# Kernel tuning notes

Hardware: AMD Instinct MI355X
Metric: run time of the kernel (lower is better)

Reference implementation:

```python
import jax, jax.numpy as jnp
import numpy as np

EMBED = 1024
HEADS = 16
HEAD_DIM = EMBED // HEADS


def setup_inputs() -> dict:
    key = jax.random.key(0)
    ks = jax.random.split(key, 8)
    N, L = 2, 2048
    s = 0.02
    return {
        "values": jax.random.normal(ks[0], (N, L, EMBED), jnp.float32),
        "keys": jax.random.normal(ks[1], (N, L, EMBED), jnp.float32),
        "queries": jax.random.normal(ks[2], (N, L, EMBED), jnp.float32),
        "Wv": jax.random.normal(ks[3], (HEAD_DIM, HEAD_DIM), jnp.float32) * s,
        "Wk": jax.random.normal(ks[4], (HEAD_DIM, HEAD_DIM), jnp.float32) * s,
        "Wq": jax.random.normal(ks[5], (HEAD_DIM, HEAD_DIM), jnp.float32) * s,
        "Wo": jax.random.normal(ks[6], (EMBED, EMBED), jnp.float32) * s,
        "bo": jnp.zeros((EMBED,), jnp.float32),
    }


def reference(values, keys, queries, Wv, Wk, Wq, Wo, bo):
    N, Lq = queries.shape[0], queries.shape[1]
    Lk = keys.shape[1]
    Lv = values.shape[1]
    # split heads: [N, L, H, D]
    v = values.reshape(N, Lv, HEADS, HEAD_DIM)
    k = keys.reshape(N, Lk, HEADS, HEAD_DIM)
    q = queries.reshape(N, Lq, HEADS, HEAD_DIM)
    # per-head linear projections (torch Linear: x @ W.T), shared across heads
    v = jnp.einsum('nlhd,ed->nlhe', v, Wv)
    k = jnp.einsum('nlhd,ed->nlhe', k, Wk)
    q = jnp.einsum('nlhd,ed->nlhe', q, Wq)
    # attention scores [N, H, Lq, Lk]
    scores = jnp.einsum('nqhd,nkhd->nhqk', q, k) / jnp.sqrt(jnp.float32(HEAD_DIM))
    attn = jax.nn.softmax(scores, axis=-1)
    out = jnp.einsum('nhql,nlhd->nqhd', attn, v).reshape(N, Lq, EMBED)
    return out @ Wo.T + bo
```

## Files before the change

kernel.cpp:

```cpp
#include <hip/hip_runtime.h>
#include <hip/hip_bf16.h>
#include <cstdint>
#include <cstddef>

#define HEADS 16
#define HDIM  64
#define EMBED 1024
#define SEQ   2048
#define NB    2

typedef __attribute__((ext_vector_type(8))) short short8;
typedef __attribute__((ext_vector_type(4))) short s16x4;
typedef __attribute__((ext_vector_type(4))) float f32x4;
typedef __attribute__((ext_vector_type(16))) float f32x16;

__device__ __forceinline__ short f2bf(float f) {
    union { float f; uint32_t u; } in{f};
    uint32_t u = in.u;
    u += 0x7fffu + ((u >> 16) & 1u);
    return (short)(u >> 16);
}

__device__ __forceinline__ int cvtpk(float a, float b) {
    __hip_bfloat162 h = __float22bfloat162_rn(make_float2(a, b));
    int i;
    __builtin_memcpy(&i, &h, 4);
    return i;
}

__device__ __forceinline__ short8 load_cvt8(const float* __restrict__ p) {
    const f32x4* q = (const f32x4*)p;
    f32x4 v0 = q[0], v1 = q[1];
    short8 r;
    r[0] = f2bf(v0[0]); r[1] = f2bf(v0[1]); r[2] = f2bf(v0[2]); r[3] = f2bf(v0[3]);
    r[4] = f2bf(v1[0]); r[5] = f2bf(v1[1]); r[6] = f2bf(v1[2]); r[7] = f2bf(v1[3]);
    return r;
}

__global__ __launch_bounds__(256) void wcvt_kernel(
    const float* __restrict__ Wq, const float* __restrict__ Wk,
    const float* __restrict__ Wv, const float* __restrict__ Wo,
    short* __restrict__ Wqb, short* __restrict__ Wkb,
    short* __restrict__ Wvb, short* __restrict__ Wob) {
    int b = blockIdx.x, tid = threadIdx.x;
    if (b < 1024) {
        int o = b * 1024 + tid * 4;
        int page = o >> 9, inp = o & 511;
        int nb = page >> 5, kb = page & 31;
        int lp = inp >> 3, jj = inp & 7;
        int row = nb * 16 + (lp & 15);
        int colf = kb * 32 + (lp >> 4) * 8 + jj;
        f32x4 v = *(const f32x4*)(Wo + row * 1024 + colf);
        s16x4 r;
        r[0] = f2bf(v[0]); r[1] = f2bf(v[1]); r[2] = f2bf(v[2]); r[3] = f2bf(v[3]);
        *(s16x4*)(Wob + o) = r;
    } else {
        const float* src = (b == 1024) ? Wq : (b == 1025) ? Wk : Wv;
        short* dst = (b == 1024) ? Wqb : (b == 1025) ? Wkb : Wvb;
        float scale = (b == 1024) ? 0.125f * 1.44269504088896341f : 1.0f;
#pragma unroll
        for (int k = 0; k < 4; ++k) {
            int idx = tid * 16 + k * 4;
            f32x4 v = *(const f32x4*)(src + idx);
            s16x4 r;
            r[0] = f2bf(v[0] * scale); r[1] = f2bf(v[1] * scale);
            r[2] = f2bf(v[2] * scale); r[3] = f2bf(v[3] * scale);
            *(s16x4*)(dst + idx) = r;
        }
    }
}

__global__ __launch_bounds__(256) void proj_kernel(
    const float* __restrict__ qrys, const float* __restrict__ keys,
    const float* __restrict__ vals,
    const short* __restrict__ Wqb, const short* __restrict__ Wkb,
    const short* __restrict__ Wvb,
    short* __restrict__ Qp, short* __restrict__ Kf, short* __restrict__ Vf) {
    __shared__ short tile[64][72];
    int tid = threadIdx.x, lane = tid & 63, w = tid >> 6;
    int g = lane >> 4, c = lane & 15;
    int tt = blockIdx.x * 64;
    int h = blockIdx.y;
    int z = blockIdx.z;
    int op = z >> 1, n = z & 1;
    int nh = n * 16 + h;
    const float* src = (op == 0) ? qrys : (op == 1) ? keys : vals;
    const short* Wb = (op == 0) ? Wqb : (op == 1) ? Wkb : Wvb;

    int lt0 = tt + w * 16;
    const float* sp_ = src + ((size_t)(n * SEQ + lt0 + c) * 16 + h) * 64;
    short8 a0 = load_cvt8(sp_ + 8 * g);
    short8 a1 = load_cvt8(sp_ + 32 + 8 * g);
#pragma unroll
    for (int ot = 0; ot < 4; ++ot) {
        short8 b0 = *(const short8*)(Wb + (ot * 16 + c) * 64 + 8 * g);
        short8 b1 = *(const short8*)(Wb + (ot * 16 + c) * 64 + 32 + 8 * g);
        f32x4 acc = {0.f, 0.f, 0.f, 0.f};
        acc = __builtin_amdgcn_mfma_f32_16x16x32_bf16(a0, b0, acc, 0, 0, 0);
        acc = __builtin_amdgcn_mfma_f32_16x16x32_bf16(a1, b1, acc, 0, 0, 0);
        if (op == 2) {
#pragma unroll
            for (int r = 0; r < 4; ++r)
                tile[ot * 16 + c][w * 16 + 4 * g + r] = f2bf(acc[r]);
        } else {
#pragma unroll
            for (int r = 0; r < 4; ++r)
                tile[w * 16 + 4 * g + r][ot * 16 + c] = f2bf(acc[r]);
        }
    }
    __syncthreads();
    if (op == 0) {
#pragma unroll
        for (int it = 0; it < 2; ++it) {
            int idx = tid + it * 256;
            int row = idx >> 3, ch = idx & 7;
            short8 v = *(const short8*)(&tile[row][ch * 8]);
            *(short8*)(Qp + ((size_t)nh * SEQ + tt + row) * 64 + ch * 8) = v;
        }
    } else {
        short* dst = (op == 1) ? Kf : Vf;
        int spx = tt >> 10;
        int tbase = (tt >> 5) & 31;
        size_t grp = (size_t)(nh * 2 + spx) * 32;
#pragma unroll
        for (int it = 0; it < 2; ++it) {
            int idx = tid + it * 256;
            int tl2 = idx >> 8;
            int p = (idx >> 6) & 3;
            int ln = idx & 63;
            int hi2 = ln >> 5, col2 = ln & 31;
            const short* srcp;
            if (op == 1) {
                srcp = &tile[tl2 * 32 + col2][p * 16 + hi2 * 8];
            } else {
                srcp = &tile[(p & 1) * 32 + col2][tl2 * 32 + (p >> 1) * 16 + hi2 * 8];
            }
            *(short8*)(dst + ((grp + tbase + tl2) * 4 + p) * 512 + ln * 8) =
                *(const short8*)srcp;
        }
    }
}

__global__ __launch_bounds__(256, 4) void attn_kernel(
    const short* __restrict__ Qp, const short* __restrict__ Kf,
    const short* __restrict__ Vf, short* __restrict__ X) {
    __shared__ float obuf[2][32][64];
    __shared__ float larr[2][2][32];

    int tid = threadIdx.x, lane = tid & 63, wave = tid >> 6;
    int col = lane & 31, hi = lane >> 5;
    int qg = wave >> 1, sp = wave & 1;

    int lid = blockIdx.x;
    int xcd = lid & 7, idx = lid >> 3;
    int nh = xcd * 4 + (idx & 3);
    int qb = idx >> 2;
    int n = nh >> 4, h = nh & 15;
    int q0w = qb * 64 + qg * 32;

    const short* Qb = Qp + (size_t)nh * SEQ * 64;
    const short* Kw = Kf + (((size_t)(nh * 2 + sp)) << 16) + lane * 8;
    const short* Vw = Vf + (((size_t)(nh * 2 + sp)) << 16) + lane * 8;

    short8 qf[4];
#pragma unroll
    for (int t = 0; t < 4; ++t)
        qf[t] = *(const short8*)(Qb + (size_t)(q0w + col) * 64 + 16 * t + 8 * hi);

    f32x16 o0, o1;
#pragma unroll
    for (int r = 0; r < 16; ++r) { o0[r] = 0.f; o1[r] = 0.f; }
    float la = 0.f, lb = 0.f;

#pragma unroll 1
    for (int t = 0; t < 32; ++t) {
        short8 kf[4], vf[4];
#pragma unroll
        for (int dt = 0; dt < 4; ++dt)
            kf[dt] = *(const short8*)(Kw + ((size_t)(t * 4 + dt) << 9));
#pragma unroll
        for (int p = 0; p < 4; ++p)
            vf[p] = *(const short8*)(Vw + ((size_t)(t * 4 + p) << 9));

        f32x16 s;
#pragma unroll
        for (int r = 0; r < 16; ++r) s[r] = 0.f;
#pragma unroll
        for (int dt = 0; dt < 4; ++dt)
            s = __builtin_amdgcn_mfma_f32_32x32x16_bf16(kf[dt], qf[dt], s, 0, 0, 0);

#pragma unroll
        for (int r = 0; r < 16; r += 2) {
            s[r] = __builtin_amdgcn_exp2f(s[r]);
            s[r + 1] = __builtin_amdgcn_exp2f(s[r + 1]);
            la += s[r];
            lb += s[r + 1];
        }
        int pk0 = cvtpk(s[0], s[1]),   pk1 = cvtpk(s[2], s[3]);
        int pk2 = cvtpk(s[4], s[5]),   pk3 = cvtpk(s[6], s[7]);
        int pk4 = cvtpk(s[8], s[9]),   pk5 = cvtpk(s[10], s[11]);
        int pk6 = cvtpk(s[12], s[13]), pk7 = cvtpk(s[14], s[15]);
        auto r02 = __builtin_amdgcn_permlane32_swap(pk0, pk2, false, false);
        auto r13 = __builtin_amdgcn_permlane32_swap(pk1, pk3, false, false);
        auto r46 = __builtin_amdgcn_permlane32_swap(pk4, pk6, false, false);
        auto r57 = __builtin_amdgcn_permlane32_swap(pk5, pk7, false, false);
        union { int i[4]; short8 s8; } pa0, pa1;
        pa0.i[0] = r02[0]; pa0.i[1] = r13[0]; pa0.i[2] = r02[1]; pa0.i[3] = r13[1];
        pa1.i[0] = r46[0]; pa1.i[1] = r57[0]; pa1.i[2] = r46[1]; pa1.i[3] = r57[1];
        o0 = __builtin_amdgcn_mfma_f32_32x32x16_bf16(pa0.s8, vf[0], o0, 0, 0, 0);
        o1 = __builtin_amdgcn_mfma_f32_32x32x16_bf16(pa0.s8, vf[1], o1, 0, 0, 0);
        o0 = __builtin_amdgcn_mfma_f32_32x32x16_bf16(pa1.s8, vf[2], o0, 0, 0, 0);
        o1 = __builtin_amdgcn_mfma_f32_32x32x16_bf16(pa1.s8, vf[3], o1, 0, 0, 0);
    }

    float l_loc = la + lb;
    l_loc += __shfl_xor(l_loc, 32);

    if (lane < 32) larr[qg][sp][col] = l_loc;
    if (sp == 0) {
#pragma unroll
        for (int r = 0; r < 16; ++r) {
            int rq = (r & 3) + 8 * (r >> 2) + 4 * hi;
            obuf[qg][rq][col] = o0[r];
            obuf[qg][rq][32 + col] = o1[r];
        }
    }
    __syncthreads();
    if (sp == 1) {
#pragma unroll
        for (int r = 0; r < 16; ++r) {
            int rq = (r & 3) + 8 * (r >> 2) + 4 * hi;
            float ltot = larr[qg][0][rq] + larr[qg][1][rq];
            float iv = 1.0f / ltot;
            float v0 = o0[r] + obuf[qg][rq][col];
            float v1 = o1[r] + obuf[qg][rq][32 + col];
            int m = n * SEQ + q0w + rq;
            size_t base = (((size_t)(m >> 4) * 32 + h * 2) << 9) +
                          (size_t)(m & 15) * 8 + ((col >> 3) << 7) + (col & 7);
            X[base] = f2bf(v0 * iv);
            X[base + 512] = f2bf(v1 * iv);
        }
    }
}

__global__ __launch_bounds__(256) void ogemm_kernel(
    const short* __restrict__ Xf, const short* __restrict__ Wf,
    const float* __restrict__ bo, float* __restrict__ out) {
    int tid = threadIdx.x, lane = tid & 63, wave = tid >> 6;
    int g = lane >> 4, c = lane & 15;
    int wr = wave >> 1, wc = wave & 1;
    int m0 = blockIdx.x * 128 + wr * 64;
    int n0 = blockIdx.y * 64 + wc * 32;

    f32x4 acc[4][2];
#pragma unroll
    for (int i = 0; i < 4; ++i)
#pragma unroll
        for (int j = 0; j < 2; ++j) acc[i][j] = (f32x4){0.f, 0.f, 0.f, 0.f};

    const short* Xp = Xf + (((size_t)(blockIdx.x * 8 + wr * 4) * 32) << 9) + lane * 8;
    const short* Wp = Wf + (((size_t)(blockIdx.y * 4 + wc * 2) * 32) << 9) + lane * 8;

    short8 a[4], b[2];
#pragma unroll
    for (int i = 0; i < 4; ++i) a[i] = *(const short8*)(Xp + ((size_t)i * 32 << 9));
#pragma unroll
    for (int j = 0; j < 2; ++j) b[j] = *(const short8*)(Wp + ((size_t)j * 32 << 9));

    for (int s = 1; s <= 32; ++s) {
        short8 an[4], bn[2];
        if (s < 32) {
#pragma unroll
            for (int i = 0; i < 4; ++i)
                an[i] = *(const short8*)(Xp + (((size_t)i * 32 + s) << 9));
#pragma unroll
            for (int j = 0; j < 2; ++j)
                bn[j] = *(const short8*)(Wp + (((size_t)j * 32 + s) << 9));
        }
#pragma unroll
        for (int i = 0; i < 4; ++i)
#pragma unroll
            for (int j = 0; j < 2; ++j)
                acc[i][j] = __builtin_amdgcn_mfma_f32_16x16x32_bf16(a[i], b[j], acc[i][j], 0, 0, 0);
        if (s < 32) {
#pragma unroll
            for (int i = 0; i < 4; ++i) a[i] = an[i];
#pragma unroll
            for (int j = 0; j < 2; ++j) b[j] = bn[j];
        }
    }

    float bias[2] = {bo[n0 + c], bo[n0 + 16 + c]};
#pragma unroll
    for (int i = 0; i < 4; ++i)
#pragma unroll
        for (int j = 0; j < 2; ++j)
#pragma unroll
            for (int r = 0; r < 4; ++r)
                out[(size_t)(m0 + i * 16 + 4 * g + r) * EMBED + n0 + j * 16 + c] =
                    acc[i][j][r] + bias[j];
}

extern "C" void kernel_launch(void* const* d_in, const int* in_sizes, int n_in,
                              void* d_out, int out_size, void* d_ws, size_t ws_size,
                              hipStream_t stream) {
    const float* vals = (const float*)d_in[0];
    const float* keys = (const float*)d_in[1];
    const float* qrys = (const float*)d_in[2];
    const float* Wv = (const float*)d_in[3];
    const float* Wk = (const float*)d_in[4];
    const float* Wq = (const float*)d_in[5];
    const float* Wo = (const float*)d_in[6];
    const float* bo = (const float*)d_in[7];
    float* out = (float*)d_out;

    char* ws = (char*)d_ws;
    const size_t sz_bf = (size_t)NB * HEADS * SEQ * HDIM * sizeof(short);
    short* Qp = (short*)(ws);
    short* Kf = (short*)(ws + sz_bf);
    short* Vf = (short*)(ws + 2 * sz_bf);
    short* X = (short*)(ws + 3 * sz_bf);
    short* Wob = (short*)(ws + 4 * sz_bf);
    short* Wqb = (short*)(ws + 4 * sz_bf + 2 * 1024 * 1024);
    short* Wkb = Wqb + 64 * 64;
    short* Wvb = Wkb + 64 * 64;

    wcvt_kernel<<<dim3(1027), dim3(256), 0, stream>>>(Wq, Wk, Wv, Wo, Wqb, Wkb, Wvb, Wob);
    proj_kernel<<<dim3(SEQ / 64, HEADS, 6), dim3(256), 0, stream>>>(
        qrys, keys, vals, Wqb, Wkb, Wvb, Qp, Kf, Vf);
    attn_kernel<<<dim3(1024), dim3(256), 0, stream>>>(Qp, Kf, Vf, X);
    ogemm_kernel<<<dim3(NB * SEQ / 128, EMBED / 64), dim3(256), 0, stream>>>(X, Wob, bo, out);
}
```

Baseline: 94.39 us.

## Move Wo bf16 conversion into attention kernel tail blocks; tidy softmax accumulators

The Wo fp32-to-bf16 repack now runs in 1024 extra blocks appended to the attention grid rather than in the weight-conversion kernel. The small Q/K/V weight kernel launches only 3 blocks, so the proj kernel is no longer held up behind the large Wo conversion, and the conversion can fill idle CUs at the end of attention. The attention loop also starts its score MFMA from a persistent zero accumulator instead of re-zeroing each iteration, and it accumulates row sums as a packed float2. The attention grid doubles in size, and the extra blocks may contend with attention blocks for bandwidth or scheduling slots.

```diff
diff --git a/kernel.cpp b/kernel.cpp
--- a/kernel.cpp
+++ b/kernel.cpp
@@ -11,6 +11,7 @@
 
 typedef __attribute__((ext_vector_type(8))) short short8;
 typedef __attribute__((ext_vector_type(4))) short s16x4;
+typedef __attribute__((ext_vector_type(2))) float f32x2;
 typedef __attribute__((ext_vector_type(4))) float f32x4;
 typedef __attribute__((ext_vector_type(16))) float f32x16;
 
@@ -39,34 +40,20 @@
 
 __global__ __launch_bounds__(256) void wcvt_kernel(
     const float* __restrict__ Wq, const float* __restrict__ Wk,
-    const float* __restrict__ Wv, const float* __restrict__ Wo,
-    short* __restrict__ Wqb, short* __restrict__ Wkb,
-    short* __restrict__ Wvb, short* __restrict__ Wob) {
+    const float* __restrict__ Wv,
+    short* __restrict__ Wqb, short* __restrict__ Wkb, short* __restrict__ Wvb) {
     int b = blockIdx.x, tid = threadIdx.x;
-    if (b < 1024) {
-        int o = b * 1024 + tid * 4;
-        int page = o >> 9, inp = o & 511;
-        int nb = page >> 5, kb = page & 31;
-        int lp = inp >> 3, jj = inp & 7;
-        int row = nb * 16 + (lp & 15);
-        int colf = kb * 32 + (lp >> 4) * 8 + jj;
-        f32x4 v = *(const f32x4*)(Wo + row * 1024 + colf);
+    const float* src = (b == 0) ? Wq : (b == 1) ? Wk : Wv;
+    short* dst = (b == 0) ? Wqb : (b == 1) ? Wkb : Wvb;
+    float scale = (b == 0) ? 0.125f * 1.44269504088896341f : 1.0f;
+#pragma unroll
+    for (int k = 0; k < 4; ++k) {
+        int idx = tid * 16 + k * 4;
+        f32x4 v = *(const f32x4*)(src + idx);
         s16x4 r;
-        r[0] = f2bf(v[0]); r[1] = f2bf(v[1]); r[2] = f2bf(v[2]); r[3] = f2bf(v[3]);
-        *(s16x4*)(Wob + o) = r;
-    } else {
-        const float* src = (b == 1024) ? Wq : (b == 1025) ? Wk : Wv;
-        short* dst = (b == 1024) ? Wqb : (b == 1025) ? Wkb : Wvb;
-        float scale = (b == 1024) ? 0.125f * 1.44269504088896341f : 1.0f;
-#pragma unroll
-        for (int k = 0; k < 4; ++k) {
-            int idx = tid * 16 + k * 4;
-            f32x4 v = *(const f32x4*)(src + idx);
-            s16x4 r;
-            r[0] = f2bf(v[0] * scale); r[1] = f2bf(v[1] * scale);
-            r[2] = f2bf(v[2] * scale); r[3] = f2bf(v[3] * scale);
-            *(s16x4*)(dst + idx) = r;
-        }
+        r[0] = f2bf(v[0] * scale); r[1] = f2bf(v[1] * scale);
+        r[2] = f2bf(v[2] * scale); r[3] = f2bf(v[3] * scale);
+        *(s16x4*)(dst + idx) = r;
     }
 }
 
@@ -143,15 +130,31 @@
 
 __global__ __launch_bounds__(256, 4) void attn_kernel(
     const short* __restrict__ Qp, const short* __restrict__ Kf,
-    const short* __restrict__ Vf, short* __restrict__ X) {
+    const short* __restrict__ Vf, short* __restrict__ X,
+    const float* __restrict__ Wo, short* __restrict__ Wob) {
     __shared__ float obuf[2][32][64];
     __shared__ float larr[2][2][32];
 
     int tid = threadIdx.x, lane = tid & 63, wave = tid >> 6;
+    int lid = blockIdx.x;
+
+    if (lid >= 1024) {
+        int o = (lid - 1024) * 1024 + tid * 4;
+        int page = o >> 9, inp = o & 511;
+        int nb = page >> 5, kb = page & 31;
+        int lp = inp >> 3, jj = inp & 7;
+        int row = nb * 16 + (lp & 15);
+        int colf = kb * 32 + (lp >> 4) * 8 + jj;
+        f32x4 v = *(const f32x4*)(Wo + row * 1024 + colf);
+        s16x4 r;
+        r[0] = f2bf(v[0]); r[1] = f2bf(v[1]); r[2] = f2bf(v[2]); r[3] = f2bf(v[3]);
+        *(s16x4*)(Wob + o) = r;
+        return;
+    }
+
     int col = lane & 31, hi = lane >> 5;
     int qg = wave >> 1, sp = wave & 1;
 
-    int lid = blockIdx.x;
     int xcd = lid & 7, idx = lid >> 3;
     int nh = xcd * 4 + (idx & 3);
     int qb = idx >> 2;
@@ -167,10 +170,10 @@
     for (int t = 0; t < 4; ++t)
         qf[t] = *(const short8*)(Qb + (size_t)(q0w + col) * 64 + 16 * t + 8 * hi);
 
-    f32x16 o0, o1;
-#pragma unroll
-    for (int r = 0; r < 16; ++r) { o0[r] = 0.f; o1[r] = 0.f; }
-    float la = 0.f, lb = 0.f;
+    f32x16 o0, o1, zac;
+#pragma unroll
+    for (int r = 0; r < 16; ++r) { o0[r] = 0.f; o1[r] = 0.f; zac[r] = 0.f; }
+    f32x2 la2 = {0.f, 0.f};
 
 #pragma unroll 1
     for (int t = 0; t < 32; ++t) {
@@ -182,19 +185,16 @@
         for (int p = 0; p < 4; ++p)
             vf[p] = *(const short8*)(Vw + ((size_t)(t * 4 + p) << 9));
 
-        f32x16 s;
-#pragma unroll
-        for (int r = 0; r < 16; ++r) s[r] = 0.f;
-#pragma unroll
-        for (int dt = 0; dt < 4; ++dt)
+        f32x16 s = __builtin_amdgcn_mfma_f32_32x32x16_bf16(kf[0], qf[0], zac, 0, 0, 0);
+#pragma unroll
+        for (int dt = 1; dt < 4; ++dt)
             s = __builtin_amdgcn_mfma_f32_32x32x16_bf16(kf[dt], qf[dt], s, 0, 0, 0);
 
 #pragma unroll
         for (int r = 0; r < 16; r += 2) {
             s[r] = __builtin_amdgcn_exp2f(s[r]);
             s[r + 1] = __builtin_amdgcn_exp2f(s[r + 1]);
-            la += s[r];
-            lb += s[r + 1];
+            la2 += (f32x2){s[r], s[r + 1]};
         }
         int pk0 = cvtpk(s[0], s[1]),   pk1 = cvtpk(s[2], s[3]);
         int pk2 = cvtpk(s[4], s[5]),   pk3 = cvtpk(s[6], s[7]);
@@ -213,7 +213,7 @@
         o1 = __builtin_amdgcn_mfma_f32_32x32x16_bf16(pa1.s8, vf[3], o1, 0, 0, 0);
     }
 
-    float l_loc = la + lb;
+    float l_loc = la2[0] + la2[1];
     l_loc += __shfl_xor(l_loc, 32);
 
     if (lane < 32) larr[qg][sp][col] = l_loc;
@@ -325,9 +325,9 @@
     short* Wkb = Wqb + 64 * 64;
     short* Wvb = Wkb + 64 * 64;
 
-    wcvt_kernel<<<dim3(1027), dim3(256), 0, stream>>>(Wq, Wk, Wv, Wo, Wqb, Wkb, Wvb, Wob);
+    wcvt_kernel<<<dim3(3), dim3(256), 0, stream>>>(Wq, Wk, Wv, Wqb, Wkb, Wvb);
     proj_kernel<<<dim3(SEQ / 64, HEADS, 6), dim3(256), 0, stream>>>(
         qrys, keys, vals, Wqb, Wkb, Wvb, Qp, Kf, Vf);
-    attn_kernel<<<dim3(1024), dim3(256), 0, stream>>>(Qp, Kf, Vf, X);
+    attn_kernel<<<dim3(2048), dim3(256), 0, stream>>>(Qp, Kf, Vf, X, Wo, Wob);
     ogemm_kernel<<<dim3(NB * SEQ / 128, EMBED / 64), dim3(256), 0, stream>>>(X, Wob, bo, out);
 }
```

Result: no change. 94.18 us (median of 3 runs) (-0.2%).
